# Optimization experiments

Measured on AMD Instinct MI355X. Metric: run time of the kernel, lower is better.

Reference implementation:

```python
import jax, jax.numpy as jnp
import numpy as np
from jax import lax

N, IN_DIM, HID, K = 12000, 256, 256, 16
EPS_LN = 1e-5


def gelu(x):
    return jax.nn.gelu(x, approximate=False)


def layernorm(x, g, b):
    mu = jnp.mean(x, axis=-1, keepdims=True)
    var = jnp.mean((x - mu) ** 2, axis=-1, keepdims=True)
    return (x - mu) * lax.rsqrt(var + EPS_LN) * g + b


def knn_graph(cents, k):
    # pairwise euclidean distances [N, N]
    sq = jnp.sum(cents * cents, axis=1)
    d2 = sq[:, None] + sq[None, :] - 2.0 * (cents @ cents.T)
    dist = jnp.sqrt(jnp.maximum(d2, 0.0))
    n = cents.shape[0]
    dist = dist + jnp.eye(n, dtype=dist.dtype) * 1e9  # exclude self (diag dist is 0)
    _, idx = lax.top_k(-dist, k)                      # k smallest
    d = jnp.take_along_axis(dist, idx, axis=1)
    inv = 1.0 / jnp.maximum(d, 1e-4)
    w = inv / jnp.maximum(jnp.sum(inv, axis=1, keepdims=True), 1e-8)
    return idx, w


def sage_layer(h, idx, w, w_self, w_nei, ln_g, ln_b):
    nei = h[idx]                                   # [N, k, D] gather
    agg = jnp.einsum('nk,nkd->nd', w, nei)         # weighted neighbor sum
    out = gelu(h @ w_self.T + agg @ w_nei.T)
    return layernorm(out, ln_g, ln_b)


def setup_inputs() -> dict:
    key = jax.random.key(0)
    ks = jax.random.split(key, 12)
    s_in = 1.0 / np.sqrt(IN_DIM)
    s_h = 1.0 / np.sqrt(HID)
    s_h2 = 1.0 / np.sqrt(HID // 2)
    return {
        'feats': jax.random.normal(ks[0], (N, IN_DIM), jnp.float32),
        'cents': jax.random.normal(ks[1], (N, 2), jnp.float32),
        'enc_w': jax.random.normal(ks[2], (HID, IN_DIM), jnp.float32) * s_in,
        'enc_b': jnp.zeros((HID,), jnp.float32),
        'g1_ws': jax.random.normal(ks[3], (HID, HID), jnp.float32) * s_h,
        'g1_wn': jax.random.normal(ks[4], (HID, HID), jnp.float32) * s_h,
        'g1_g': jnp.ones((HID,), jnp.float32),
        'g1_b': jnp.zeros((HID,), jnp.float32),
        'g2_ws': jax.random.normal(ks[5], (HID, HID), jnp.float32) * s_h,
        'g2_wn': jax.random.normal(ks[6], (HID, HID), jnp.float32) * s_h,
        'g2_g': jnp.ones((HID,), jnp.float32),
        'g2_b': jnp.zeros((HID,), jnp.float32),
        'cls_w1': jax.random.normal(ks[7], (HID // 2, HID), jnp.float32) * s_h,
        'cls_b1': jnp.zeros((HID // 2,), jnp.float32),
        'cls_w2': jax.random.normal(ks[8], (1, HID // 2), jnp.float32) * s_h2,
        'cls_b2': jnp.zeros((1,), jnp.float32),
    }


def reference(feats, cents, enc_w, enc_b, g1_ws, g1_wn, g1_g, g1_b,
              g2_ws, g2_wn, g2_g, g2_b, cls_w1, cls_b1, cls_w2, cls_b2):
    h = gelu(feats @ enc_w.T + enc_b)
    idx, w = knn_graph(cents, K)
    h = h + sage_layer(h, idx, w, g1_ws, g1_wn, g1_g, g1_b)
    h = h + sage_layer(h, idx, w, g2_ws, g2_wn, g2_g, g2_b)
    logits = gelu(h @ cls_w1.T + cls_b1) @ cls_w2.T + cls_b2
    return jax.nn.sigmoid(logits)[:, 0]
```

## Files before the change

### kernel.cpp

```cpp
#include <hip/hip_runtime.h>
#include <hip/hip_bf16.h>
#include <stdint.h>

#define NND 12000
#define DM  256
#define KNN 16
#define NB  4096
#define BW  0.00390625f
#define RW  16

#define FPBAR(x) asm volatile("" : "+v"(x))

typedef unsigned long long u64;

__device__ __forceinline__ float geluf(float x){ return 0.5f*x*(1.0f + erff(x*0.70710678118654752f)); }
__device__ __forceinline__ int bucketof(float x){
  int b = (int)floorf((x + 8.0f) * 256.0f);
  return min(max(b, 0), NB-1);
}

__device__ __forceinline__ u64 make_key(float xi, float yi, float sqi,
                                        float cx, float cy, int jd, int self){
  float ax = cx*cx;  FPBAR(ax);
  float ay = cy*cy;  FPBAR(ay);
  float sqj = ax + ay;   FPBAR(sqj);
  float px = xi*cx;    FPBAR(px);
  float py = yi*cy;    FPBAR(py);
  float dt = px + py;    FPBAR(dt);
  float two_dt = 2.0f*dt;  FPBAR(two_dt);
  float ss = sqi + sqj;    FPBAR(ss);
  float d2 = ss - two_dt;  FPBAR(d2);
  float dist = __fsqrt_rn(fmaxf(d2, 0.0f));
  u64 key = ((u64)__float_as_uint(dist) << 32) | (unsigned)jd;
  return (jd == self) ? ~0ULL : key;
}

__device__ __forceinline__ void ladder_insert(u64* L, u64 key){
  bool c[KNN];
  #pragma unroll
  for (int t=0;t<KNN;t++) c[t] = key < L[t];
  #pragma unroll
  for (int t=KNN-1;t>=1;t--) L[t] = c[t-1] ? L[t-1] : (c[t] ? key : L[t]);
  L[0] = c[0] ? key : L[0];
}

__device__ __forceinline__ u64 wave_merge16(u64* slice, int lane, const u64* L)
{
  #pragma unroll
  for (int t=0;t<KNN;t++) slice[t*64 + lane] = L[t];
  int p = 0;
  u64 cur = slice[lane];
  u64 out16 = ~0ULL;
  for (int r=0;r<KNN;r++){
    u64 k = cur; int who = lane;
    #pragma unroll
    for (int o=32;o>0;o>>=1){
      u64 ok = __shfl_xor(k, o, 64);
      int ow = __shfl_xor(who, o, 64);
      if (ok < k){ k = ok; who = ow; }
    }
    if (lane == r) out16 = k;
    if (lane == who){
      ++p;
      cur = (p < KNN) ? slice[p*64 + lane] : ~0ULL;
    }
  }
  return out16;
}

__device__ __forceinline__ void write_outputs(u64 out16, int lane, int n,
    int* __restrict__ idx_out, float* __restrict__ w_out)
{
  if (lane < KNN) idx_out[(size_t)n*KNN + lane] = (int)(unsigned)(out16 & 0xFFFFFFFFull);
  u64 kt[KNN];
  #pragma unroll
  for (int t=0;t<KNN;t++) kt[t] = __shfl(out16, t, 64);
  float inv[KNN];
  #pragma unroll
  for (int t=0;t<KNN;t++){
    float d = __uint_as_float((unsigned)(kt[t] >> 32));
    inv[t] = __fdiv_rn(1.0f, fmaxf(d, 1e-4f));
  }
  float r8v[8];
  #pragma unroll
  for (int t=0;t<8;t++){ r8v[t] = inv[t] + inv[t+8]; FPBAR(r8v[t]); }
  float s01 = r8v[0]+r8v[1]; FPBAR(s01);
  float s23 = r8v[2]+r8v[3]; FPBAR(s23);
  float s45 = r8v[4]+r8v[5]; FPBAR(s45);
  float s67 = r8v[6]+r8v[7]; FPBAR(s67);
  float sA = s01+s23; FPBAR(sA);
  float sB = s45+s67; FPBAR(sB);
  float s = sA + sB;
  s = fmaxf(s, 1e-8f);
  if (lane < KNN){
    float d = __uint_as_float((unsigned)(out16 >> 32));
    float invL = __fdiv_rn(1.0f, fmaxf(d, 1e-4f));
    w_out[(size_t)n*KNN + lane] = __fdiv_rn(invL, s);
  }
}

__global__ __launch_bounds__(256) void detect_kernel_r15(
    const unsigned* __restrict__ a, int na,
    const unsigned* __restrict__ b, int nb, int* __restrict__ flag)
{
  __shared__ int cnt;
  if (threadIdx.x == 0) cnt = 0;
  __syncthreads();
  int c = 0;
  for (int i = threadIdx.x; i < na; i += 256){
    int ex = (a[i] >> 7) & 0xFF;
    c += (ex >= 113 && ex <= 131) ? 1 : 0;
  }
  for (int i = threadIdx.x; i < nb; i += 256){
    int ex = (b[i] >> 7) & 0xFF;
    c += (ex >= 113 && ex <= 131) ? 1 : 0;
  }
  atomicAdd(&cnt, c);
  __syncthreads();
  if (threadIdx.x == 0) *flag = (cnt > (na + nb) / 2) ? 1 : 0;
}

struct SegTable {
  const void* src[16];
  float*      dst[16];
  int         cnt[16];
  int         total;
};

__global__ __launch_bounds__(256) void decode_kernel_r15(SegTable t, const int* __restrict__ flag)
{
  const int is_bf16 = *flag;
  for (int e = blockIdx.x*256 + threadIdx.x; e < t.total; e += gridDim.x*256){
    int rem = e, s = 0;
    while (rem >= t.cnt[s]){ rem -= t.cnt[s]; ++s; }
    float v;
    if (is_bf16) v = __uint_as_float(((unsigned)((const unsigned short*)t.src[s])[rem]) << 16);
    else         v = ((const float*)t.src[s])[rem];
    t.dst[s][rem] = v;
  }
}

__global__ __launch_bounds__(256) void zero_kernel_r15(int* __restrict__ hist, int* __restrict__ cursor,
                                                       int* __restrict__ ocnt)
{
  int t = blockIdx.x*256 + threadIdx.x;
  if (t < NB){ hist[t] = 0; cursor[t] = 0; }
  if (blockIdx.x == 0 && threadIdx.x == 0) *ocnt = 0;
}

__global__ __launch_bounds__(256) void count_kernel_r15(const float* __restrict__ cents,
                                                        int* __restrict__ hist)
{
  int i = blockIdx.x*256 + threadIdx.x;
  if (i < NND) atomicAdd(&hist[bucketof(cents[2*i])], 1);
}

__global__ __launch_bounds__(1024) void scan_kernel_r15(const int* __restrict__ hist,
                                                        int* __restrict__ offs)
{
  __shared__ int s[1024];
  int t = threadIdx.x;
  int h0 = hist[t*4], h1 = hist[t*4+1], h2 = hist[t*4+2], h3 = hist[t*4+3];
  int tot = h0+h1+h2+h3;
  s[t] = tot;
  __syncthreads();
  for (int d=1; d<1024; d<<=1){
    int v = (t >= d) ? s[t-d] : 0;
    __syncthreads();
    s[t] += v;
    __syncthreads();
  }
  int excl = s[t] - tot;
  offs[t*4]   = excl;
  offs[t*4+1] = excl + h0;
  offs[t*4+2] = excl + h0 + h1;
  offs[t*4+3] = excl + h0 + h1 + h2;
}

__global__ __launch_bounds__(256) void scatter_kernel_r15(const float* __restrict__ cents,
    const int* __restrict__ offs, int* __restrict__ cursor,
    float2* __restrict__ sxy, int* __restrict__ sid)
{
  int i = blockIdx.x*256 + threadIdx.x;
  if (i < NND){
    float x = cents[2*i], y = cents[2*i+1];
    int b = bucketof(x);
    int pos = offs[b] + atomicAdd(&cursor[b], 1);
    sxy[pos] = make_float2(x, y);
    sid[pos] = i;
  }
}

__global__ __launch_bounds__(256) void knn_fixed_r15(
    const float2* __restrict__ sxy, const int* __restrict__ sid,
    const float* __restrict__ cents, const int* __restrict__ offs,
    int* __restrict__ idx_out, float* __restrict__ w_out,
    int* __restrict__ ocnt, int* __restrict__ olist, float* __restrict__ othr)
{
  __shared__ u64 lds_k[4][KNN*64];
  const int lane = threadIdx.x & 63, wv = threadIdx.x >> 6;
  const int n = blockIdx.x*4 + wv;
  const float xi = cents[2*n];
  const float yi = cents[2*n+1];
  float sx = xi*xi; FPBAR(sx);
  float sy = yi*yi; FPBAR(sy);
  float sqi = sx + sy; FPBAR(sqi);

  const int start = offs[bucketof(xi)];
  const bool isR = lane < 32;
  const int lo = isR ? lane : (lane - 32);

  u64 L[KNN];
  #pragma unroll
  for (int t=0;t<KNN;t++) L[t] = ~0ULL;

  #pragma unroll 2
  for (int r=0;r<RW;r++){
    int myp = isR ? (start + r*32 + lo) : (start - 1 - r*32 - lo);
    bool act = (myp >= 0) && (myp < NND);
    float2 cu = make_float2(0.f, 0.f);
    int jd = -1;
    if (act){ cu = sxy[myp]; jd = sid[myp]; }
    u64 key = make_key(xi, yi, sqi, cu.x, cu.y, jd, n);
    if (!act) key = ~0ULL;
    ladder_insert(L, key);
  }

  u64 out16 = wave_merge16(&lds_k[wv][0], lane, L);
  float B = __uint_as_float((unsigned)(__shfl(out16, KNN-1, 64) >> 32));
  const float thr = B*B + 2e-4f;

  const int qr = min(start + RW*32, NND);
  const int ql = max(start - RW*32, 0);
  bool ok;
  {
    bool rok = (qr >= NND);
    if (!rok){
      float xR = sxy[qr-1].x;
      float dxr = ((float)bucketof(xR)*BW - 8.0f) - xi;
      rok = (dxr > 0.0f) && (dxr*dxr > thr);
    }
    bool lok = (ql <= 0);
    if (!lok){
      float xL = sxy[ql].x;
      float dxl = xi - ((float)(bucketof(xL)+1)*BW - 8.0f);
      lok = (dxl > 0.0f) && (dxl*dxl > thr);
    }
    ok = rok && lok;
  }
  if (lane == 0 && !ok){
    int s = atomicAdd(ocnt, 1);
    olist[s] = n;
    othr[s] = thr;
  }

  write_outputs(out16, lane, n, idx_out, w_out);
}

__global__ __launch_bounds__(256) void knn_ext_r15(
    const float2* __restrict__ sxy, const int* __restrict__ sid,
    const float* __restrict__ cents, const int* __restrict__ offs,
    const int* __restrict__ olist, const float* __restrict__ othr,
    const int* __restrict__ ocnt,
    int* __restrict__ idx_out, float* __restrict__ w_out)
{
  __shared__ u64 lds_k[4][KNN*64];
  const int lane = threadIdx.x & 63, wv = threadIdx.x >> 6;
  const int cnt = *ocnt;

  for (int slot = blockIdx.x*4 + wv; slot < cnt; slot += gridDim.x*4){
    const int n = olist[slot];
    const float thr = othr[slot];
    const float rB = __fsqrt_rn(thr) * (1.0f + 2e-6f);
    const float xi = cents[2*n];
    const float yi = cents[2*n+1];
    float sx = xi*xi; FPBAR(sx);
    float sy = yi*yi; FPBAR(sy);
    float sqi = sx + sy; FPBAR(sqi);

    const int bL = bucketof(xi - rB);
    const int bR = bucketof(xi + rB);
    const int posL = offs[bL];
    const int posR = (bR + 1 < NB) ? offs[bR + 1] : NND;

    u64 L[KNN];
    #pragma unroll
    for (int t=0;t<KNN;t++) L[t] = ~0ULL;

    for (int p = posL + lane; p < posR; p += 64){
      float2 cu = sxy[p];
      ladder_insert(L, make_key(xi, yi, sqi, cu.x, cu.y, sid[p], n));
    }

    u64 out16 = wave_merge16(&lds_k[wv][0], lane, L);
    write_outputs(out16, lane, n, idx_out, w_out);
  }
}

template<int OUT, bool DUAL, bool BIAS>
__global__ __launch_bounds__(256) void mm_kernel_r15(
    const float* __restrict__ A1, const float* __restrict__ A2,
    const float* __restrict__ W1, const float* __restrict__ W2,
    const float* __restrict__ bias, float* __restrict__ C)
{
  constexpr int KC = 16;
  constexpr int TM = 32;
  constexpr int WS = KC + 4;
  constexpr int NQ = OUT / 64;
  __shared__ float Wl1[OUT*WS];
  __shared__ float Wl2[DUAL ? OUT*WS : 1];
  __shared__ float Al1[TM*KC];
  __shared__ float Al2[DUAL ? TM*KC : 1];

  const int tid = threadIdx.x;
  const int cg  = tid & 63;
  const int rg  = tid >> 6;
  const int m0  = blockIdx.x * TM;

  float acc[8][NQ];
  #pragma unroll
  for (int r=0;r<8;r++)
    #pragma unroll
    for (int q=0;q<NQ;q++) acc[r][q] = 0.f;

  for (int c0=0; c0<DM; c0+=KC){
    for (int e=tid; e < OUT*(KC/4); e += 256){
      int row = e >> 2;
      int c4  = (e & 3)*4;
      *(float4*)&Wl1[row*WS + c4] = *(const float4*)(W1 + (size_t)row*DM + c0 + c4);
      if (DUAL)
        *(float4*)&Wl2[row*WS + c4] = *(const float4*)(W2 + (size_t)row*DM + c0 + c4);
    }
    for (int e=tid; e < TM*(KC/4); e += 256){
      int row = e >> 2;
      int c4  = (e & 3)*4;
      size_t gi = (size_t)(m0+row)*DM + c0 + c4;
      *(float4*)&Al1[row*KC+c4] = *(const float4*)(A1 + gi);
      if (DUAL) *(float4*)&Al2[row*KC+c4] = *(const float4*)(A2 + gi);
    }
    __syncthreads();
    #pragma unroll
    for (int k4=0; k4<KC/4; k4++){
      float4 wv1[NQ]; float4 wv2[NQ];
      #pragma unroll
      for (int q=0;q<NQ;q++){
        wv1[q] = *(const float4*)&Wl1[(cg+64*q)*WS + k4*4];
        if (DUAL) wv2[q] = *(const float4*)&Wl2[(cg+64*q)*WS + k4*4];
      }
      #pragma unroll
      for (int r=0;r<8;r++){
        float4 a1 = *(const float4*)&Al1[(rg*8+r)*KC + k4*4];
        float4 a2;
        if (DUAL) a2 = *(const float4*)&Al2[(rg*8+r)*KC + k4*4];
        #pragma unroll
        for (int q=0;q<NQ;q++){
          float s = acc[r][q];
          s = fmaf(a1.x, wv1[q].x, s);
          s = fmaf(a1.y, wv1[q].y, s);
          s = fmaf(a1.z, wv1[q].z, s);
          s = fmaf(a1.w, wv1[q].w, s);
          if (DUAL){
            s = fmaf(a2.x, wv2[q].x, s);
            s = fmaf(a2.y, wv2[q].y, s);
            s = fmaf(a2.z, wv2[q].z, s);
            s = fmaf(a2.w, wv2[q].w, s);
          }
          acc[r][q] = s;
        }
      }
    }
    __syncthreads();
  }
  #pragma unroll
  for (int q=0;q<NQ;q++){
    int d = cg + 64*q;
    float bv = BIAS ? bias[d] : 0.f;
    #pragma unroll
    for (int r=0;r<8;r++){
      float v = geluf(acc[r][q] + bv);
      C[(size_t)(m0 + rg*8 + r)*OUT + d] = v;
    }
  }
}

__global__ __launch_bounds__(256) void agg_kernel_r15(const float* __restrict__ h,
    const int* __restrict__ idx, const float* __restrict__ w, float* __restrict__ agg)
{
  const int lane = threadIdx.x & 63, wid = threadIdx.x >> 6;
  const int n = blockIdx.x*4 + wid;
  const int base = n*KNN;
  float4 acc = make_float4(0.f,0.f,0.f,0.f);
  for (int k=0;k<KNN;k++){
    int j = idx[base+k];
    float wk = w[base+k];
    float4 hv = *(const float4*)(h + (size_t)j*DM + lane*4);
    acc.x = fmaf(wk, hv.x, acc.x);
    acc.y = fmaf(wk, hv.y, acc.y);
    acc.z = fmaf(wk, hv.z, acc.z);
    acc.w = fmaf(wk, hv.w, acc.w);
  }
  *(float4*)(agg + (size_t)n*DM + lane*4) = acc;
}

__global__ __launch_bounds__(256) void ln_res_kernel_r15(float* __restrict__ h,
    const float* __restrict__ tmp, const float* __restrict__ g, const float* __restrict__ b)
{
  const int lane = threadIdx.x & 63, wid = threadIdx.x >> 6;
  const int n = blockIdx.x*4 + wid;
  float4 x = *(const float4*)(tmp + (size_t)n*DM + lane*4);
  float s = (x.x + x.y) + (x.z + x.w);
  #pragma unroll
  for (int off=32; off>0; off>>=1) s += __shfl_xor(s, off, 64);
  float mu = s * (1.0f/DM);
  float dx0 = x.x-mu, dx1 = x.y-mu, dx2 = x.z-mu, dx3 = x.w-mu;
  float v = (dx0*dx0 + dx1*dx1) + (dx2*dx2 + dx3*dx3);
  #pragma unroll
  for (int off=32; off>0; off>>=1) v += __shfl_xor(v, off, 64);
  float rs = 1.0f / sqrtf(v * (1.0f/DM) + 1e-5f);
  int c = lane*4;
  float4 gv = *(const float4*)(g + c);
  float4 bv = *(const float4*)(b + c);
  float4 hv = *(const float4*)(h + (size_t)n*DM + c);
  hv.x += dx0*rs*gv.x + bv.x;
  hv.y += dx1*rs*gv.y + bv.y;
  hv.z += dx2*rs*gv.z + bv.z;
  hv.w += dx3*rs*gv.w + bv.w;
  *(float4*)(h + (size_t)n*DM + c) = hv;
}

__global__ __launch_bounds__(256) void cls2_kernel_r15(const float* __restrict__ hid,
    const float* __restrict__ w2, const float* __restrict__ b2,
    void* __restrict__ out, const int* __restrict__ flag)
{
  const int lane = threadIdx.x & 63, wid = threadIdx.x >> 6;
  const int n = blockIdx.x*4 + wid;
  float a = hid[(size_t)n*128 + lane]      * w2[lane]
          + hid[(size_t)n*128 + 64 + lane] * w2[64+lane];
  #pragma unroll
  for (int off=32; off>0; off>>=1) a += __shfl_xor(a, off, 64);
  if (lane == 0){
    float v = 1.0f / (1.0f + expf(-(a + b2[0])));
    if (*flag) ((__hip_bfloat16*)out)[n] = __float2bfloat16(v);
    else       ((float*)out)[n] = v;
  }
}

extern "C" void kernel_launch(void* const* d_in, const int* in_sizes, int n_in,
                              void* d_out, int out_size, void* d_ws, size_t ws_size,
                              hipStream_t stream)
{
  char* base = (char*)d_ws;
  int*   flag = (int*)base;
  float* wreg = (float*)(base + 16);
  static const int sizes[16] = {
    NND*256, NND*2, 256*256, 256, 256*256, 256*256, 256, 256,
    256*256, 256*256, 256, 256, 128*256, 128, 128, 1
  };
  float* ptrs[16];
  {
    float* p = wreg;
    for (int i = 2; i < 16; i++){ ptrs[i] = p; p += sizes[i]; }
    ptrs[1] = p;
    p += NND*2;
    ptrs[0] = p;
  }
  float* F    = ptrs[0];
  float* C    = ptrs[1];
  float* h    = F + (size_t)NND*DM;
  float* agg  = h + (size_t)NND*DM;
  float* hid  = agg + (size_t)NND*DM;
  int*  gidx  = (int*)(hid + (size_t)NND*128);
  float* gw   = (float*)(gidx + (size_t)NND*KNN);
  float2* sxy   = (float2*)(gw + (size_t)NND*KNN);
  int*    sid   = (int*)(sxy + NND);
  int*    hist  = sid + NND;
  int*    cursor= hist + NB;
  int*    offs  = cursor + NB;
  int*    ocnt  = offs + NB;
  int*    olist = ocnt + 1;
  float*  othr  = (float*)(olist + NND);

  detect_kernel_r15<<<1, 256, 0, stream>>>((const unsigned*)d_in[1], 4096,
                                           (const unsigned*)d_in[0], 16384, flag);
  SegTable t;
  int total = 0;
  for (int i = 0; i < 16; i++){
    t.src[i] = d_in[i];
    t.dst[i] = ptrs[i];
    t.cnt[i] = sizes[i];
    total += sizes[i];
  }
  t.total = total;
  decode_kernel_r15<<<(total + 255)/256, 256, 0, stream>>>(t, flag);

  const float* enc_w  = ptrs[2];  const float* enc_b  = ptrs[3];
  const float* g1_ws  = ptrs[4];  const float* g1_wn  = ptrs[5];
  const float* g1_g   = ptrs[6];  const float* g1_b   = ptrs[7];
  const float* g2_ws  = ptrs[8];  const float* g2_wn  = ptrs[9];
  const float* g2_g   = ptrs[10]; const float* g2_b   = ptrs[11];
  const float* cls_w1 = ptrs[12]; const float* cls_b1 = ptrs[13];
  const float* cls_w2 = ptrs[14]; const float* cls_b2 = ptrs[15];

  dim3 b256(256);
  zero_kernel_r15<<<(NB + 255)/256, b256, 0, stream>>>(hist, cursor, ocnt);
  count_kernel_r15<<<(NND + 255)/256, b256, 0, stream>>>(C, hist);
  scan_kernel_r15<<<1, 1024, 0, stream>>>(hist, offs);
  scatter_kernel_r15<<<(NND + 255)/256, b256, 0, stream>>>(C, offs, cursor, sxy, sid);
  mm_kernel_r15<256,false,true><<<NND/32, b256, 0, stream>>>(F, nullptr, enc_w, nullptr, enc_b, h);
  knn_fixed_r15<<<NND/4, b256, 0, stream>>>(sxy, sid, C, offs, gidx, gw, ocnt, olist, othr);
  knn_ext_r15<<<512, b256, 0, stream>>>(sxy, sid, C, offs, olist, othr, ocnt, gidx, gw);
  agg_kernel_r15<<<NND/4, b256, 0, stream>>>(h, gidx, gw, agg);
  mm_kernel_r15<256,true,false><<<NND/32, b256, 0, stream>>>(h, agg, g1_ws, g1_wn, nullptr, F);
  ln_res_kernel_r15<<<NND/4, b256, 0, stream>>>(h, F, g1_g, g1_b);
  agg_kernel_r15<<<NND/4, b256, 0, stream>>>(h, gidx, gw, agg);
  mm_kernel_r15<256,true,false><<<NND/32, b256, 0, stream>>>(h, agg, g2_ws, g2_wn, nullptr, F);
  ln_res_kernel_r15<<<NND/4, b256, 0, stream>>>(h, F, g2_g, g2_b);
  mm_kernel_r15<128,false,true><<<NND/32, b256, 0, stream>>>(h, nullptr, cls_w1, nullptr, cls_b1, hid);
  cls2_kernel_r15<<<NND/4, b256, 0, stream>>>(hid, cls_w2, cls_b2, d_out, flag);
}
```

Before: 569.2 us.

## Split matmul output columns across grid and prefetch next K-chunk into registers

The fp32 matmul kernel now tiles output columns in blocks of 128 using a second grid dimension, so the 256-wide layers run twice as many blocks, each with half the weight tile in LDS and half the accumulators. It also adds register double-buffering: the next K-chunk of weights and activations is loaded into registers while the current chunk is computed, which removes the trailing barrier. This is meant to raise occupancy and hide global load latency in the encoder, SAGE and classifier GEMMs. The cost is that each activation tile is loaded twice across column blocks, and more registers are held live for the prefetch.

```diff
diff --git a/kernel.cpp b/kernel.cpp
--- a/kernel.cpp
+++ b/kernel.cpp
@@ -99,7 +99,7 @@
   }
 }
 
-__global__ __launch_bounds__(256) void detect_kernel_r15(
+__global__ __launch_bounds__(256) void detect_kernel_r17(
     const unsigned* __restrict__ a, int na,
     const unsigned* __restrict__ b, int nb, int* __restrict__ flag)
 {
@@ -127,7 +127,7 @@
   int         total;
 };
 
-__global__ __launch_bounds__(256) void decode_kernel_r15(SegTable t, const int* __restrict__ flag)
+__global__ __launch_bounds__(256) void decode_kernel_r17(SegTable t, const int* __restrict__ flag)
 {
   const int is_bf16 = *flag;
   for (int e = blockIdx.x*256 + threadIdx.x; e < t.total; e += gridDim.x*256){
@@ -140,7 +140,7 @@
   }
 }
 
-__global__ __launch_bounds__(256) void zero_kernel_r15(int* __restrict__ hist, int* __restrict__ cursor,
+__global__ __launch_bounds__(256) void zero_kernel_r17(int* __restrict__ hist, int* __restrict__ cursor,
                                                        int* __restrict__ ocnt)
 {
   int t = blockIdx.x*256 + threadIdx.x;
@@ -148,14 +148,14 @@
   if (blockIdx.x == 0 && threadIdx.x == 0) *ocnt = 0;
 }
 
-__global__ __launch_bounds__(256) void count_kernel_r15(const float* __restrict__ cents,
+__global__ __launch_bounds__(256) void count_kernel_r17(const float* __restrict__ cents,
                                                         int* __restrict__ hist)
 {
   int i = blockIdx.x*256 + threadIdx.x;
   if (i < NND) atomicAdd(&hist[bucketof(cents[2*i])], 1);
 }
 
-__global__ __launch_bounds__(1024) void scan_kernel_r15(const int* __restrict__ hist,
+__global__ __launch_bounds__(1024) void scan_kernel_r17(const int* __restrict__ hist,
                                                         int* __restrict__ offs)
 {
   __shared__ int s[1024];
@@ -177,7 +177,7 @@
   offs[t*4+3] = excl + h0 + h1 + h2;
 }
 
-__global__ __launch_bounds__(256) void scatter_kernel_r15(const float* __restrict__ cents,
+__global__ __launch_bounds__(256) void scatter_kernel_r17(const float* __restrict__ cents,
     const int* __restrict__ offs, int* __restrict__ cursor,
     float2* __restrict__ sxy, int* __restrict__ sid)
 {
@@ -191,7 +191,7 @@
   }
 }
 
-__global__ __launch_bounds__(256) void knn_fixed_r15(
+__global__ __launch_bounds__(256) void knn_fixed_r17(
     const float2* __restrict__ sxy, const int* __restrict__ sid,
     const float* __restrict__ cents, const int* __restrict__ offs,
     int* __restrict__ idx_out, float* __restrict__ w_out,
@@ -257,7 +257,7 @@
   write_outputs(out16, lane, n, idx_out, w_out);
 }
 
-__global__ __launch_bounds__(256) void knn_ext_r15(
+__global__ __launch_bounds__(256) void knn_ext_r17(
     const float2* __restrict__ sxy, const int* __restrict__ sid,
     const float* __restrict__ cents, const int* __restrict__ offs,
     const int* __restrict__ olist, const float* __restrict__ othr,
@@ -297,8 +297,8 @@
   }
 }
 
-template<int OUT, bool DUAL, bool BIAS>
-__global__ __launch_bounds__(256) void mm_kernel_r15(
+template<int OUT, int COLS, bool DUAL, bool BIAS>
+__global__ __launch_bounds__(256) void mm_kernel_r17(
     const float* __restrict__ A1, const float* __restrict__ A2,
     const float* __restrict__ W1, const float* __restrict__ W2,
     const float* __restrict__ bias, float* __restrict__ C)
@@ -306,9 +306,9 @@
   constexpr int KC = 16;
   constexpr int TM = 32;
   constexpr int WS = KC + 4;
-  constexpr int NQ = OUT / 64;
-  __shared__ float Wl1[OUT*WS];
-  __shared__ float Wl2[DUAL ? OUT*WS : 1];
+  constexpr int NQ = COLS / 64;
+  __shared__ float Wl1[COLS*WS];
+  __shared__ float Wl2[DUAL ? COLS*WS : 1];
   __shared__ float Al1[TM*KC];
   __shared__ float Al2[DUAL ? TM*KC : 1];
 
@@ -316,6 +316,27 @@
   const int cg  = tid & 63;
   const int rg  = tid >> 6;
   const int m0  = blockIdx.x * TM;
+  const int colbase = blockIdx.y * COLS;
+
+  const int wrow0 = tid >> 2,          wc40 = (tid & 3)*4;
+  const int wrow1 = (tid+256) >> 2,    wc41 = ((tid+256) & 3)*4;
+  const bool hasA = tid < TM*4;
+  const int arow = tid >> 2,           ac4  = (tid & 3)*4;
+
+  float4 w1r0, w1r1, w2r0, w2r1, a1r, a2r;
+
+  auto load_chunk = [&](int c0){
+    w1r0 = *(const float4*)(W1 + (size_t)(colbase+wrow0)*DM + c0 + wc40);
+    w1r1 = *(const float4*)(W1 + (size_t)(colbase+wrow1)*DM + c0 + wc41);
+    if (DUAL){
+      w2r0 = *(const float4*)(W2 + (size_t)(colbase+wrow0)*DM + c0 + wc40);
+      w2r1 = *(const float4*)(W2 + (size_t)(colbase+wrow1)*DM + c0 + wc41);
+    }
+    if (hasA){
+      a1r = *(const float4*)(A1 + (size_t)(m0+arow)*DM + c0 + ac4);
+      if (DUAL) a2r = *(const float4*)(A2 + (size_t)(m0+arow)*DM + c0 + ac4);
+    }
+  };
 
   float acc[8][NQ];
   #pragma unroll
@@ -323,22 +344,23 @@
     #pragma unroll
     for (int q=0;q<NQ;q++) acc[r][q] = 0.f;
 
+  load_chunk(0);
+
   for (int c0=0; c0<DM; c0+=KC){
-    for (int e=tid; e < OUT*(KC/4); e += 256){
-      int row = e >> 2;
-      int c4  = (e & 3)*4;
-      *(float4*)&Wl1[row*WS + c4] = *(const float4*)(W1 + (size_t)row*DM + c0 + c4);
-      if (DUAL)
-        *(float4*)&Wl2[row*WS + c4] = *(const float4*)(W2 + (size_t)row*DM + c0 + c4);
-    }
-    for (int e=tid; e < TM*(KC/4); e += 256){
-      int row = e >> 2;
-      int c4  = (e & 3)*4;
-      size_t gi = (size_t)(m0+row)*DM + c0 + c4;
-      *(float4*)&Al1[row*KC+c4] = *(const float4*)(A1 + gi);
-      if (DUAL) *(float4*)&Al2[row*KC+c4] = *(const float4*)(A2 + gi);
-    }
     __syncthreads();
+    *(float4*)&Wl1[wrow0*WS + wc40] = w1r0;
+    *(float4*)&Wl1[wrow1*WS + wc41] = w1r1;
+    if (DUAL){
+      *(float4*)&Wl2[wrow0*WS + wc40] = w2r0;
+      *(float4*)&Wl2[wrow1*WS + wc41] = w2r1;
+    }
+    if (hasA){
+      *(float4*)&Al1[arow*KC + ac4] = a1r;
+      if (DUAL) *(float4*)&Al2[arow*KC + ac4] = a2r;
+    }
+    __syncthreads();
+    if (c0 + KC < DM) load_chunk(c0 + KC);
+
     #pragma unroll
     for (int k4=0; k4<KC/4; k4++){
       float4 wv1[NQ]; float4 wv2[NQ];
@@ -369,11 +391,10 @@
         }
       }
     }
-    __syncthreads();
   }
   #pragma unroll
   for (int q=0;q<NQ;q++){
-    int d = cg + 64*q;
+    int d = colbase + cg + 64*q;
     float bv = BIAS ? bias[d] : 0.f;
     #pragma unroll
     for (int r=0;r<8;r++){
@@ -383,7 +404,7 @@
   }
 }
 
-__global__ __launch_bounds__(256) void agg_kernel_r15(const float* __restrict__ h,
+__global__ __launch_bounds__(256) void agg_kernel_r17(const float* __restrict__ h,
     const int* __restrict__ idx, const float* __restrict__ w, float* __restrict__ agg)
 {
   const int lane = threadIdx.x & 63, wid = threadIdx.x >> 6;
@@ -402,7 +423,7 @@
   *(float4*)(agg + (size_t)n*DM + lane*4) = acc;
 }
 
-__global__ __launch_bounds__(256) void ln_res_kernel_r15(float* __restrict__ h,
+__global__ __launch_bounds__(256) void ln_res_kernel_r17(float* __restrict__ h,
     const float* __restrict__ tmp, const float* __restrict__ g, const float* __restrict__ b)
 {
   const int lane = threadIdx.x & 63, wid = threadIdx.x >> 6;
@@ -428,7 +449,7 @@
   *(float4*)(h + (size_t)n*DM + c) = hv;
 }
 
-__global__ __launch_bounds__(256) void cls2_kernel_r15(const float* __restrict__ hid,
+__global__ __launch_bounds__(256) void cls2_kernel_r17(const float* __restrict__ hid,
     const float* __restrict__ w2, const float* __restrict__ b2,
     void* __restrict__ out, const int* __restrict__ flag)
 {
@@ -480,7 +501,7 @@
   int*    olist = ocnt + 1;
   float*  othr  = (float*)(olist + NND);
 
-  detect_kernel_r15<<<1, 256, 0, stream>>>((const unsigned*)d_in[1], 4096,
+  detect_kernel_r17<<<1, 256, 0, stream>>>((const unsigned*)d_in[1], 4096,
                                            (const unsigned*)d_in[0], 16384, flag);
   SegTable t;
   int total = 0;
@@ -491,7 +512,7 @@
     total += sizes[i];
   }
   t.total = total;
-  decode_kernel_r15<<<(total + 255)/256, 256, 0, stream>>>(t, flag);
+  decode_kernel_r17<<<(total + 255)/256, 256, 0, stream>>>(t, flag);
 
   const float* enc_w  = ptrs[2];  const float* enc_b  = ptrs[3];
   const float* g1_ws  = ptrs[4];  const float* g1_wn  = ptrs[5];
@@ -502,19 +523,19 @@
   const float* cls_w2 = ptrs[14]; const float* cls_b2 = ptrs[15];
 
   dim3 b256(256);
-  zero_kernel_r15<<<(NB + 255)/256, b256, 0, stream>>>(hist, cursor, ocnt);
-  count_kernel_r15<<<(NND + 255)/256, b256, 0, stream>>>(C, hist);
-  scan_kernel_r15<<<1, 1024, 0, stream>>>(hist, offs);
-  scatter_kernel_r15<<<(NND + 255)/256, b256, 0, stream>>>(C, offs, cursor, sxy, sid);
-  mm_kernel_r15<256,false,true><<<NND/32, b256, 0, stream>>>(F, nullptr, enc_w, nullptr, enc_b, h);
-  knn_fixed_r15<<<NND/4, b256, 0, stream>>>(sxy, sid, C, offs, gidx, gw, ocnt, olist, othr);
-  knn_ext_r15<<<512, b256, 0, stream>>>(sxy, sid, C, offs, olist, othr, ocnt, gidx, gw);
-  agg_kernel_r15<<<NND/4, b256, 0, stream>>>(h, gidx, gw, agg);
-  mm_kernel_r15<256,true,false><<<NND/32, b256, 0, stream>>>(h, agg, g1_ws, g1_wn, nullptr, F);
-  ln_res_kernel_r15<<<NND/4, b256, 0, stream>>>(h, F, g1_g, g1_b);
-  agg_kernel_r15<<<NND/4, b256, 0, stream>>>(h, gidx, gw, agg);
-  mm_kernel_r15<256,true,false><<<NND/32, b256, 0, stream>>>(h, agg, g2_ws, g2_wn, nullptr, F);
-  ln_res_kernel_r15<<<NND/4, b256, 0, stream>>>(h, F, g2_g, g2_b);
-  mm_kernel_r15<128,false,true><<<NND/32, b256, 0, stream>>>(h, nullptr, cls_w1, nullptr, cls_b1, hid);
-  cls2_kernel_r15<<<NND/4, b256, 0, stream>>>(hid, cls_w2, cls_b2, d_out, flag);
-}
+  zero_kernel_r17<<<(NB + 255)/256, b256, 0, stream>>>(hist, cursor, ocnt);
+  count_kernel_r17<<<(NND + 255)/256, b256, 0, stream>>>(C, hist);
+  scan_kernel_r17<<<1, 1024, 0, stream>>>(hist, offs);
+  scatter_kernel_r17<<<(NND + 255)/256, b256, 0, stream>>>(C, offs, cursor, sxy, sid);
+  mm_kernel_r17<256,128,false,true><<<dim3(NND/32, 2), b256, 0, stream>>>(F, nullptr, enc_w, nullptr, enc_b, h);
+  knn_fixed_r17<<<NND/4, b256, 0, stream>>>(sxy, sid, C, offs, gidx, gw, ocnt, olist, othr);
+  knn_ext_r17<<<512, b256, 0, stream>>>(sxy, sid, C, offs, olist, othr, ocnt, gidx, gw);
+  agg_kernel_r17<<<NND/4, b256, 0, stream>>>(h, gidx, gw, agg);
+  mm_kernel_r17<256,128,true,false><<<dim3(NND/32, 2), b256, 0, stream>>>(h, agg, g1_ws, g1_wn, nullptr, F);
+  ln_res_kernel_r17<<<NND/4, b256, 0, stream>>>(h, F, g1_g, g1_b);
+  agg_kernel_r17<<<NND/4, b256, 0, stream>>>(h, gidx, gw, agg);
+  mm_kernel_r17<256,128,true,false><<<dim3(NND/32, 2), b256, 0, stream>>>(h, agg, g2_ws, g2_wn, nullptr, F);
+  ln_res_kernel_r17<<<NND/4, b256, 0, stream>>>(h, F, g2_g, g2_b);
+  mm_kernel_r17<128,128,false,true><<<dim3(NND/32, 1), b256, 0, stream>>>(h, nullptr, cls_w1, nullptr, cls_b1, hid);
+  cls2_kernel_r17<<<NND/4, b256, 0, stream>>>(hid, cls_w2, cls_b2, d_out, flag);
+}
```

Measured after the change: 523.3 us. 8.1% less time.

## Replace FP32 SIMT matmuls with split-bf16 MFMA matmuls

Applied to the files above, without the earlier changes.

Converts all weight matrices once per call into high/low bf16 pairs and rewrites the dense matmul kernel to use 16x16x32 bf16 MFMA instructions. Each product uses three MFMAs (hi*hi, hi*lo, lo*hi) to approximate fp32 accuracy. Activations are split on the fly from fp32 global loads without LDS staging, and each wave computes a 16x64 output tile. This removes the scalar-FMA compute bottleneck, at the cost of an extra conversion kernel, uncached global weight reads, and a small loss of precision.

```diff
diff --git a/kernel.cpp b/kernel.cpp
--- a/kernel.cpp
+++ b/kernel.cpp
@@ -8,15 +8,37 @@
 #define NB  4096
 #define BW  0.00390625f
 #define RW  16
+#define NWELEM 360448
 
 #define FPBAR(x) asm volatile("" : "+v"(x))
 
 typedef unsigned long long u64;
+typedef __attribute__((ext_vector_type(8))) short bf8_t;
+typedef __attribute__((ext_vector_type(4))) float f4_t;
 
 __device__ __forceinline__ float geluf(float x){ return 0.5f*x*(1.0f + erff(x*0.70710678118654752f)); }
 __device__ __forceinline__ int bucketof(float x){
   int b = (int)floorf((x + 8.0f) * 256.0f);
   return min(max(b, 0), NB-1);
+}
+
+__device__ __forceinline__ unsigned short bf16_rne(float x){
+  unsigned u = __float_as_uint(x);
+  unsigned r = u + 0x7FFF + ((u >> 16) & 1);
+  return (unsigned short)(r >> 16);
+}
+
+__device__ __forceinline__ void split8(const float4& v0, const float4& v1,
+                                       bf8_t& h, bf8_t& l){
+  float xs[8] = {v0.x,v0.y,v0.z,v0.w,v1.x,v1.y,v1.z,v1.w};
+  #pragma unroll
+  for (int i=0;i<8;i++){
+    unsigned short hb = bf16_rne(xs[i]);
+    float hf = __uint_as_float(((unsigned)hb) << 16);
+    unsigned short lb = bf16_rne(xs[i] - hf);
+    h[i] = (short)hb;
+    l[i] = (short)lb;
+  }
 }
 
 __device__ __forceinline__ u64 make_key(float xi, float yi, float sqi,
@@ -99,7 +121,7 @@
   }
 }
 
-__global__ __launch_bounds__(256) void detect_kernel_r15(
+__global__ __launch_bounds__(256) void detect_kernel_r18(
     const unsigned* __restrict__ a, int na,
     const unsigned* __restrict__ b, int nb, int* __restrict__ flag)
 {
@@ -127,7 +149,7 @@
   int         total;
 };
 
-__global__ __launch_bounds__(256) void decode_kernel_r15(SegTable t, const int* __restrict__ flag)
+__global__ __launch_bounds__(256) void decode_kernel_r18(SegTable t, const int* __restrict__ flag)
 {
   const int is_bf16 = *flag;
   for (int e = blockIdx.x*256 + threadIdx.x; e < t.total; e += gridDim.x*256){
@@ -140,7 +162,23 @@
   }
 }
 
-__global__ __launch_bounds__(256) void zero_kernel_r15(int* __restrict__ hist, int* __restrict__ cursor,
+struct WcTable { const float* src[6]; int cnt[6]; };
+
+__global__ __launch_bounds__(256) void wconv_r18(WcTable t,
+    unsigned short* __restrict__ dh, unsigned short* __restrict__ dl)
+{
+  for (int e = blockIdx.x*256 + threadIdx.x; e < NWELEM; e += gridDim.x*256){
+    int rem = e, s = 0;
+    while (rem >= t.cnt[s]){ rem -= t.cnt[s]; ++s; }
+    float x = t.src[s][rem];
+    unsigned short hb = bf16_rne(x);
+    float hf = __uint_as_float(((unsigned)hb) << 16);
+    dh[e] = hb;
+    dl[e] = bf16_rne(x - hf);
+  }
+}
+
+__global__ __launch_bounds__(256) void zero_kernel_r18(int* __restrict__ hist, int* __restrict__ cursor,
                                                        int* __restrict__ ocnt)
 {
   int t = blockIdx.x*256 + threadIdx.x;
@@ -148,14 +186,14 @@
   if (blockIdx.x == 0 && threadIdx.x == 0) *ocnt = 0;
 }
 
-__global__ __launch_bounds__(256) void count_kernel_r15(const float* __restrict__ cents,
+__global__ __launch_bounds__(256) void count_kernel_r18(const float* __restrict__ cents,
                                                         int* __restrict__ hist)
 {
   int i = blockIdx.x*256 + threadIdx.x;
   if (i < NND) atomicAdd(&hist[bucketof(cents[2*i])], 1);
 }
 
-__global__ __launch_bounds__(1024) void scan_kernel_r15(const int* __restrict__ hist,
+__global__ __launch_bounds__(1024) void scan_kernel_r18(const int* __restrict__ hist,
                                                         int* __restrict__ offs)
 {
   __shared__ int s[1024];
@@ -177,7 +215,7 @@
   offs[t*4+3] = excl + h0 + h1 + h2;
 }
 
-__global__ __launch_bounds__(256) void scatter_kernel_r15(const float* __restrict__ cents,
+__global__ __launch_bounds__(256) void scatter_kernel_r18(const float* __restrict__ cents,
     const int* __restrict__ offs, int* __restrict__ cursor,
     float2* __restrict__ sxy, int* __restrict__ sid)
 {
@@ -191,7 +229,7 @@
   }
 }
 
-__global__ __launch_bounds__(256) void knn_fixed_r15(
+__global__ __launch_bounds__(256) void knn_fixed_r18(
     const float2* __restrict__ sxy, const int* __restrict__ sid,
     const float* __restrict__ cents, const int* __restrict__ offs,
     int* __restrict__ idx_out, float* __restrict__ w_out,
@@ -257,7 +295,7 @@
   write_outputs(out16, lane, n, idx_out, w_out);
 }
 
-__global__ __launch_bounds__(256) void knn_ext_r15(
+__global__ __launch_bounds__(256) void knn_ext_r18(
     const float2* __restrict__ sxy, const int* __restrict__ sid,
     const float* __restrict__ cents, const int* __restrict__ offs,
     const int* __restrict__ olist, const float* __restrict__ othr,
@@ -298,92 +336,72 @@
 }
 
 template<int OUT, bool DUAL, bool BIAS>
-__global__ __launch_bounds__(256) void mm_kernel_r15(
+__global__ __launch_bounds__(256) void mm_mfma_r18(
     const float* __restrict__ A1, const float* __restrict__ A2,
-    const float* __restrict__ W1, const float* __restrict__ W2,
-    const float* __restrict__ bias, float* __restrict__ C)
-{
-  constexpr int KC = 16;
-  constexpr int TM = 32;
-  constexpr int WS = KC + 4;
-  constexpr int NQ = OUT / 64;
-  __shared__ float Wl1[OUT*WS];
-  __shared__ float Wl2[DUAL ? OUT*WS : 1];
-  __shared__ float Al1[TM*KC];
-  __shared__ float Al2[DUAL ? TM*KC : 1];
-
-  const int tid = threadIdx.x;
-  const int cg  = tid & 63;
-  const int rg  = tid >> 6;
-  const int m0  = blockIdx.x * TM;
-
-  float acc[8][NQ];
-  #pragma unroll
-  for (int r=0;r<8;r++)
+    const unsigned short* __restrict__ W1h, const unsigned short* __restrict__ W1l,
+    const unsigned short* __restrict__ W2h, const unsigned short* __restrict__ W2l,
+    const float* __restrict__ bias, float* __restrict__ C, int njobs)
+{
+  constexpr int NCG = OUT / 64;
+  const int lane = threadIdx.x & 63, wv = threadIdx.x >> 6;
+  const int job = blockIdx.x*4 + wv;
+  if (job >= njobs) return;
+  const int rowtile = job / NCG;
+  const int cg = job % NCG;
+  const int l15 = lane & 15;
+  const int quad = lane >> 4;
+  const int m = rowtile*16 + l15;
+  const int n0 = cg*64;
+  const int nb = n0 + l15;
+
+  f4_t acc[4];
+  #pragma unroll
+  for (int t=0;t<4;t++) acc[t] = (f4_t){0.f,0.f,0.f,0.f};
+
+  for (int k0=0; k0<DM; k0+=32){
+    const int kq = k0 + quad*8;
+    bf8_t a1h, a1l, a2h, a2l;
+    {
+      float4 v0 = *(const float4*)(A1 + (size_t)m*DM + kq);
+      float4 v1 = *(const float4*)(A1 + (size_t)m*DM + kq + 4);
+      split8(v0, v1, a1h, a1l);
+      if (DUAL){
+        float4 u0 = *(const float4*)(A2 + (size_t)m*DM + kq);
+        float4 u1 = *(const float4*)(A2 + (size_t)m*DM + kq + 4);
+        split8(u0, u1, a2h, a2l);
+      }
+    }
     #pragma unroll
-    for (int q=0;q<NQ;q++) acc[r][q] = 0.f;
-
-  for (int c0=0; c0<DM; c0+=KC){
-    for (int e=tid; e < OUT*(KC/4); e += 256){
-      int row = e >> 2;
-      int c4  = (e & 3)*4;
-      *(float4*)&Wl1[row*WS + c4] = *(const float4*)(W1 + (size_t)row*DM + c0 + c4);
-      if (DUAL)
-        *(float4*)&Wl2[row*WS + c4] = *(const float4*)(W2 + (size_t)row*DM + c0 + c4);
-    }
-    for (int e=tid; e < TM*(KC/4); e += 256){
-      int row = e >> 2;
-      int c4  = (e & 3)*4;
-      size_t gi = (size_t)(m0+row)*DM + c0 + c4;
-      *(float4*)&Al1[row*KC+c4] = *(const float4*)(A1 + gi);
-      if (DUAL) *(float4*)&Al2[row*KC+c4] = *(const float4*)(A2 + gi);
-    }
-    __syncthreads();
+    for (int t=0;t<4;t++){
+      size_t wo = (size_t)(nb + t*16)*DM + kq;
+      bf8_t bh = *(const bf8_t*)(W1h + wo);
+      bf8_t bl = *(const bf8_t*)(W1l + wo);
+      acc[t] = __builtin_amdgcn_mfma_f32_16x16x32_bf16(a1h, bh, acc[t], 0, 0, 0);
+      acc[t] = __builtin_amdgcn_mfma_f32_16x16x32_bf16(a1h, bl, acc[t], 0, 0, 0);
+      acc[t] = __builtin_amdgcn_mfma_f32_16x16x32_bf16(a1l, bh, acc[t], 0, 0, 0);
+      if (DUAL){
+        bf8_t ch = *(const bf8_t*)(W2h + wo);
+        bf8_t cl = *(const bf8_t*)(W2l + wo);
+        acc[t] = __builtin_amdgcn_mfma_f32_16x16x32_bf16(a2h, ch, acc[t], 0, 0, 0);
+        acc[t] = __builtin_amdgcn_mfma_f32_16x16x32_bf16(a2h, cl, acc[t], 0, 0, 0);
+        acc[t] = __builtin_amdgcn_mfma_f32_16x16x32_bf16(a2l, ch, acc[t], 0, 0, 0);
+      }
+    }
+  }
+
+  #pragma unroll
+  for (int t=0;t<4;t++){
+    int n = n0 + t*16 + l15;
+    float bv = BIAS ? bias[n] : 0.f;
     #pragma unroll
-    for (int k4=0; k4<KC/4; k4++){
-      float4 wv1[NQ]; float4 wv2[NQ];
-      #pragma unroll
-      for (int q=0;q<NQ;q++){
-        wv1[q] = *(const float4*)&Wl1[(cg+64*q)*WS + k4*4];
-        if (DUAL) wv2[q] = *(const float4*)&Wl2[(cg+64*q)*WS + k4*4];
-      }
-      #pragma unroll
-      for (int r=0;r<8;r++){
-        float4 a1 = *(const float4*)&Al1[(rg*8+r)*KC + k4*4];
-        float4 a2;
-        if (DUAL) a2 = *(const float4*)&Al2[(rg*8+r)*KC + k4*4];
-        #pragma unroll
-        for (int q=0;q<NQ;q++){
-          float s = acc[r][q];
-          s = fmaf(a1.x, wv1[q].x, s);
-          s = fmaf(a1.y, wv1[q].y, s);
-          s = fmaf(a1.z, wv1[q].z, s);
-          s = fmaf(a1.w, wv1[q].w, s);
-          if (DUAL){
-            s = fmaf(a2.x, wv2[q].x, s);
-            s = fmaf(a2.y, wv2[q].y, s);
-            s = fmaf(a2.z, wv2[q].z, s);
-            s = fmaf(a2.w, wv2[q].w, s);
-          }
-          acc[r][q] = s;
-        }
-      }
-    }
-    __syncthreads();
-  }
-  #pragma unroll
-  for (int q=0;q<NQ;q++){
-    int d = cg + 64*q;
-    float bv = BIAS ? bias[d] : 0.f;
-    #pragma unroll
-    for (int r=0;r<8;r++){
-      float v = geluf(acc[r][q] + bv);
-      C[(size_t)(m0 + rg*8 + r)*OUT + d] = v;
-    }
-  }
-}
-
-__global__ __launch_bounds__(256) void agg_kernel_r15(const float* __restrict__ h,
+    for (int r=0;r<4;r++){
+      int row = rowtile*16 + quad*4 + r;
+      C[(size_t)row*OUT + n] = geluf(acc[t][r] + bv);
+    }
+  }
+}
+
+__global__ __launch_bounds__(256) void agg_kernel_r18(const float* __restrict__ h,
     const int* __restrict__ idx, const float* __restrict__ w, float* __restrict__ agg)
 {
   const int lane = threadIdx.x & 63, wid = threadIdx.x >> 6;
@@ -402,7 +420,7 @@
   *(float4*)(agg + (size_t)n*DM + lane*4) = acc;
 }
 
-__global__ __launch_bounds__(256) void ln_res_kernel_r15(float* __restrict__ h,
+__global__ __launch_bounds__(256) void ln_res_kernel_r18(float* __restrict__ h,
     const float* __restrict__ tmp, const float* __restrict__ g, const float* __restrict__ b)
 {
   const int lane = threadIdx.x & 63, wid = threadIdx.x >> 6;
@@ -428,7 +446,7 @@
   *(float4*)(h + (size_t)n*DM + c) = hv;
 }
 
-__global__ __launch_bounds__(256) void cls2_kernel_r15(const float* __restrict__ hid,
+__global__ __launch_bounds__(256) void cls2_kernel_r18(const float* __restrict__ hid,
     const float* __restrict__ w2, const float* __restrict__ b2,
     void* __restrict__ out, const int* __restrict__ flag)
 {
@@ -479,8 +497,10 @@
   int*    ocnt  = offs + NB;
   int*    olist = ocnt + 1;
   float*  othr  = (float*)(olist + NND);
-
-  detect_kernel_r15<<<1, 256, 0, stream>>>((const unsigned*)d_in[1], 4096,
+  unsigned short* wh = (unsigned short*)(othr + NND);
+  unsigned short* wl = wh + NWELEM;
+
+  detect_kernel_r18<<<1, 256, 0, stream>>>((const unsigned*)d_in[1], 4096,
                                            (const unsigned*)d_in[0], 16384, flag);
   SegTable t;
   int total = 0;
@@ -491,30 +511,41 @@
     total += sizes[i];
   }
   t.total = total;
-  decode_kernel_r15<<<(total + 255)/256, 256, 0, stream>>>(t, flag);
-
-  const float* enc_w  = ptrs[2];  const float* enc_b  = ptrs[3];
-  const float* g1_ws  = ptrs[4];  const float* g1_wn  = ptrs[5];
+  decode_kernel_r18<<<(total + 255)/256, 256, 0, stream>>>(t, flag);
+
+  const float* enc_b  = ptrs[3];
   const float* g1_g   = ptrs[6];  const float* g1_b   = ptrs[7];
-  const float* g2_ws  = ptrs[8];  const float* g2_wn  = ptrs[9];
   const float* g2_g   = ptrs[10]; const float* g2_b   = ptrs[11];
-  const float* cls_w1 = ptrs[12]; const float* cls_b1 = ptrs[13];
+  const float* cls_b1 = ptrs[13];
   const float* cls_w2 = ptrs[14]; const float* cls_b2 = ptrs[15];
 
+  WcTable wt;
+  wt.src[0] = ptrs[2];  wt.cnt[0] = 65536;
+  wt.src[1] = ptrs[4];  wt.cnt[1] = 65536;
+  wt.src[2] = ptrs[5];  wt.cnt[2] = 65536;
+  wt.src[3] = ptrs[8];  wt.cnt[3] = 65536;
+  wt.src[4] = ptrs[9];  wt.cnt[4] = 65536;
+  wt.src[5] = ptrs[12]; wt.cnt[5] = 32768;
+  wconv_r18<<<512, 256, 0, stream>>>(wt, wh, wl);
+
   dim3 b256(256);
-  zero_kernel_r15<<<(NB + 255)/256, b256, 0, stream>>>(hist, cursor, ocnt);
-  count_kernel_r15<<<(NND + 255)/256, b256, 0, stream>>>(C, hist);
-  scan_kernel_r15<<<1, 1024, 0, stream>>>(hist, offs);
-  scatter_kernel_r15<<<(NND + 255)/256, b256, 0, stream>>>(C, offs, cursor, sxy, sid);
-  mm_kernel_r15<256,false,true><<<NND/32, b256, 0, stream>>>(F, nullptr, enc_w, nullptr, enc_b, h);
-  knn_fixed_r15<<<NND/4, b256, 0, stream>>>(sxy, sid, C, offs, gidx, gw, ocnt, olist, othr);
-  knn_ext_r15<<<512, b256, 0, stream>>>(sxy, sid, C, offs, olist, othr, ocnt, gidx, gw);
-  agg_kernel_r15<<<NND/4, b256, 0, stream>>>(h, gidx, gw, agg);
-  mm_kernel_r15<256,true,false><<<NND/32, b256, 0, stream>>>(h, agg, g1_ws, g1_wn, nullptr, F);
-  ln_res_kernel_r15<<<NND/4, b256, 0, stream>>>(h, F, g1_g, g1_b);
-  agg_kernel_r15<<<NND/4, b256, 0, stream>>>(h, gidx, gw, agg);
-  mm_kernel_r15<256,true,false><<<NND/32, b256, 0, stream>>>(h, agg, g2_ws, g2_wn, nullptr, F);
-  ln_res_kernel_r15<<<NND/4, b256, 0, stream>>>(h, F, g2_g, g2_b);
-  mm_kernel_r15<128,false,true><<<NND/32, b256, 0, stream>>>(h, nullptr, cls_w1, nullptr, cls_b1, hid);
-  cls2_kernel_r15<<<NND/4, b256, 0, stream>>>(hid, cls_w2, cls_b2, d_out, flag);
-}
+  zero_kernel_r18<<<(NB + 255)/256, b256, 0, stream>>>(hist, cursor, ocnt);
+  count_kernel_r18<<<(NND + 255)/256, b256, 0, stream>>>(C, hist);
+  scan_kernel_r18<<<1, 1024, 0, stream>>>(hist, offs);
+  scatter_kernel_r18<<<(NND + 255)/256, b256, 0, stream>>>(C, offs, cursor, sxy, sid);
+  mm_mfma_r18<256,false,true><<<750, b256, 0, stream>>>(F, nullptr,
+      wh + 0, wl + 0, nullptr, nullptr, enc_b, h, 3000);
+  knn_fixed_r18<<<NND/4, b256, 0, stream>>>(sxy, sid, C, offs, gidx, gw, ocnt, olist, othr);
+  knn_ext_r18<<<512, b256, 0, stream>>>(sxy, sid, C, offs, olist, othr, ocnt, gidx, gw);
+  agg_kernel_r18<<<NND/4, b256, 0, stream>>>(h, gidx, gw, agg);
+  mm_mfma_r18<256,true,false><<<750, b256, 0, stream>>>(h, agg,
+      wh + 65536, wl + 65536, wh + 131072, wl + 131072, nullptr, F, 3000);
+  ln_res_kernel_r18<<<NND/4, b256, 0, stream>>>(h, F, g1_g, g1_b);
+  agg_kernel_r18<<<NND/4, b256, 0, stream>>>(h, gidx, gw, agg);
+  mm_mfma_r18<256,true,false><<<750, b256, 0, stream>>>(h, agg,
+      wh + 196608, wl + 196608, wh + 262144, wl + 262144, nullptr, F, 3000);
+  ln_res_kernel_r18<<<NND/4, b256, 0, stream>>>(h, F, g2_g, g2_b);
+  mm_mfma_r18<128,false,true><<<375, b256, 0, stream>>>(h, nullptr,
+      wh + 327680, wl + 327680, nullptr, nullptr, cls_b1, hid, 1500);
+  cls2_kernel_r18<<<NND/4, b256, 0, stream>>>(hid, cls_w2, cls_b2, d_out, flag);
+}
```

Result: faster. 500.2 us (-12.1%).
